# Optimization experiments

Measured on AMD Instinct MI355X. Metric: run time of the kernel, lower is better.

## Reference

```python
import jax, jax.numpy as jnp
import numpy as np

NUM_BASES = 8
DEGREE = 3
KSIZE = 3
DOMAIN = (0.0, 1.0)


def bspline_basis(x, degree, knots):
    """Cox-de Boor recursion, vectorized over all elements of x.
    x: [...] float; knots: [num_bases + degree + 1].
    Returns basis values of shape [..., num_bases].
    (The original torch code evaluates this same recursion per-tap inside
    nested loops; here it is evaluated once, batched, with correct knot
    index bookkeeping. Uniform distinct knots -> no zero denominators.)
    """
    xe = x[..., None]  # [..., 1]
    # degree-0: indicator of each knot interval -> [..., L-1]
    B = ((knots[:-1] <= xe) & (xe < knots[1:])).astype(x.dtype)
    for d in range(1, degree + 1):
        left = (xe - knots[:-(d + 1)]) / (knots[d:-1] - knots[:-(d + 1)]) * B[..., :-1]
        right = (knots[d + 1:] - xe) / (knots[d + 1:] - knots[1:-d]) * B[..., 1:]
        B = left + right  # [..., L-d-1]
    return B  # [..., num_bases]


def setup_inputs() -> dict:
    key = jax.random.key(0)
    k1, k2 = jax.random.split(key)
    # inputs uniform in [0,1) so they lie inside the B-spline domain
    x = jax.random.uniform(k1, (16, 64, 64, 64), dtype=jnp.float32)
    # per-tap spline coefficients: [Cout, Cin, K, K, num_bases]
    coeff = jax.random.normal(k2, (64, 64, KSIZE, KSIZE, NUM_BASES), dtype=jnp.float32)
    return {"x": x, "coeff": coeff}


def reference(x, coeff):
    # normalize to domain (identity for domain=(0,1), kept for faithfulness)
    xn = (x - DOMAIN[0]) / (DOMAIN[1] - DOMAIN[0])
    knots = jnp.linspace(DOMAIN[0], DOMAIN[1], NUM_BASES + DEGREE + 1, dtype=x.dtype)
    # spline basis for every input element: [B, Cin, H, W, nb]
    phi = bspline_basis(xn, DEGREE, knots)
    Bn, Cin, H, W, nb = phi.shape
    Cout = coeff.shape[0]
    # The KAN conv  out[b,o,h,w] = sum_{j,k,l,m} phi[b,j,h+k,w+l,m]*coeff[o,j,k,l,m]
    # is exactly a VALID conv with Cin*nb input channels.
    phi_c = jnp.transpose(phi, (0, 1, 4, 2, 3)).reshape(Bn, Cin * nb, H, W)
    w = jnp.transpose(coeff, (0, 1, 4, 2, 3)).reshape(Cout, Cin * nb, KSIZE, KSIZE)
    out = jax.lax.conv_general_dilated(
        phi_c, w, window_strides=(1, 1), padding="VALID",
        dimension_numbers=("NCHW", "OIHW", "NCHW"))
    return out  # [B, Cout, H-K+1, W-K+1]
```

## Files before the change

### kernel.cpp

```cpp
#include <hip/hip_runtime.h>
#include <hip/hip_bf16.h>


typedef short v8s __attribute__((ext_vector_type(8)));
typedef float v4f __attribute__((ext_vector_type(4)));
typedef float v16f __attribute__((ext_vector_type(16)));
typedef unsigned long long u64;
typedef u64 v2u64 __attribute__((ext_vector_type(2)));

#define B_N   16
#define CIN   64
#define COUT  64
#define H_IN  64
#define W_IN  64
#define NB    8
#define HO    62
#define WO    62
#define JC    8
#define NCH   8

__device__ __forceinline__ ushort f2bf(float f) {
    uint xu = __float_as_uint(f);
    return (ushort)((xu + 0x7fffu + ((xu >> 16) & 1u)) >> 16);
}

__device__ __forceinline__ uint cvtpk(float a, float b) {
    uint r;
    asm("v_cvt_pk_bf16_f32 %0, %1, %2" : "=v"(r) : "v"(a), "v"(b));
    return r;
}

__global__ void prep_coeff_kernel(const float* __restrict__ coeff, ushort* __restrict__ bt) {
    int n = blockIdx.x * 256 + threadIdx.x;
    if (n >= 294912) return;
    int m  = n & 7;
    int g2 = (n >> 3) & 1;
    int o  = (n >> 4) & 63;
    int jp = (n >> 10) & 3;
    int q  = n >> 12;
    int tap = q % 9;
    int jc  = q / 9;
    int j = jc * 8 + jp * 2 + g2;
    bt[n] = f2bf(coeff[((o * CIN + j) * 9 + tap) * 8 + m]);
}

#define MFMA32(a, b, c) __builtin_amdgcn_mfma_f32_32x32x16_bf16((a), (b), (c), 0, 0, 0)
#define MFMA16(a, b, c) __builtin_amdgcn_mfma_f32_16x16x32_bf16((a), (b), (c), 0, 0, 0)

__global__ __launch_bounds__(256, 4) void kan_conv_ks3(
        const float* __restrict__ x, const ushort* __restrict__ cb,
        float* __restrict__ out) {
    const int h    = blockIdx.x;
    const int b    = blockIdx.y;
    const int tid  = threadIdx.x;
    const int lane = tid & 63;
    const int kh   = tid >> 6;
    const int l31  = lane & 31;
    const int g2   = lane >> 5;

    __shared__ __align__(16) char smraw[32768];

    char* wrB = smraw + kh * 6144 + lane * 16;
    const char* rdB = smraw + kh * 6144 + g2 * 1024 + l31 * 16;

    v16f acc[2][2];
    acc[0][0] = (v16f)(0.f); acc[0][1] = (v16f)(0.f);
    acc[1][0] = (v16f)(0.f); acc[1][1] = (v16f)(0.f);

    float xr0[6], xr1[6];
    const float* xb = x + ((size_t)(b * CIN) * H_IN + h) * W_IN + lane;
    const int jx = kh * 2;

#define XL(dst, jcn) { \
    _Pragma("unroll") \
    for (int e = 0; e < 6; ++e) \
        dst[e] = xb[(size_t)((jcn) * 8 + jx + (e & 1)) * (H_IN * W_IN) + (e >> 1) * W_IN]; \
    }

    auto PW = [&](float xval, int e) {
        float s_ = xval * 11.0f;
        int i0 = (int)s_;
        i0 = i0 < 0 ? 0 : (i0 > 10 ? 10 : i0);
        float u  = s_ - (float)i0;
        float um = 1.0f - u;
        float u2 = u * u, u3 = u2 * u;
        const float inv6 = 1.0f / 6.0f;
        float n0 = um * um * um * inv6;
        float n1 = (3.0f * u3 - 6.0f * u2 + 4.0f) * inv6;
        float n2 = (-3.0f * u3 + 3.0f * u2 + 3.0f * u + 1.0f) * inv6;
        float n3 = u3 * inv6;
        u64 V = (u64)cvtpk(n0, n1) | ((u64)cvtpk(n2, n3) << 32);
        int bi = i0 - 3;
        u64 lo = bi < 0 ? (V >> (uint)(-16 * bi))
               : bi < 4 ? (V << (uint)(16 * bi)) : 0ull;
        u64 hi = bi <= 0 ? 0ull
               : bi < 4 ? (V >> (uint)(64 - 16 * bi))
               : (V << (uint)(16 * bi - 64));
        v2u64 pk; pk[0] = lo; pk[1] = hi;
        *reinterpret_cast<v2u64*>(wrB + e * 1024) = pk;
    };
    auto TAP = [&](const char* pAc, int k, int lt, int tap) {
        v8s b0 = *reinterpret_cast<const v8s*>(rdB + k * 2048 + lt * 16);
        v8s b1 = *reinterpret_cast<const v8s*>(rdB + k * 2048 + 512 + lt * 16);
        v8s a0 = *reinterpret_cast<const v8s*>(pAc + tap * 8192);
        v8s a1 = *reinterpret_cast<const v8s*>(pAc + tap * 8192 + 1024);
        acc[0][0] = MFMA32(a0, b0, acc[0][0]);
        acc[0][1] = MFMA32(a0, b1, acc[0][1]);
        acc[1][0] = MFMA32(a1, b0, acc[1][0]);
        acc[1][1] = MFMA32(a1, b1, acc[1][1]);
    };

    const char* pA = (const char*)cb + (size_t)(kh * 128 + l31 * 2 + g2) * 16;

    XL(xr0, 0);
    PW(xr0[0], 0); PW(xr0[1], 1); PW(xr0[2], 2);
    PW(xr0[3], 3); PW(xr0[4], 4); PW(xr0[5], 5);
    XL(xr1, 1);

#define CHUNK(jc, CUR, NXT) { \
    const char* pAc = pA + (size_t)(jc) * 73728; \
    TAP(pAc, 0, 0, 0); \
    TAP(pAc, 0, 1, 1); \
    if ((jc) + 2 < NCH) XL(NXT, (jc) + 2); \
    TAP(pAc, 0, 2, 2); \
    if ((jc) + 1 < NCH) { PW(CUR[0], 0); PW(CUR[1], 1); } \
    TAP(pAc, 1, 0, 3); \
    TAP(pAc, 1, 1, 4); \
    TAP(pAc, 1, 2, 5); \
    if ((jc) + 1 < NCH) { PW(CUR[2], 2); PW(CUR[3], 3); } \
    TAP(pAc, 2, 0, 6); \
    TAP(pAc, 2, 1, 7); \
    TAP(pAc, 2, 2, 8); \
    if ((jc) + 1 < NCH) { PW(CUR[4], 4); PW(CUR[5], 5); } \
    }

    for (int jj = 0; jj < 4; ++jj) {
        CHUNK(2 * jj,     xr1, xr0);
        CHUNK(2 * jj + 1, xr0, xr1);
    }

#define WR_FULL(off) { \
    _Pragma("unroll") \
    for (int t = 0; t < 4; ++t) { \
        _Pragma("unroll") \
        for (int q = 0; q < 4; ++q) { \
            v4f v; \
            _Pragma("unroll") \
            for (int z = 0; z < 4; ++z) v[z] = acc[t >> 1][t & 1][q * 4 + z]; \
            *reinterpret_cast<v4f*>(smraw + (off) + (t * 4 + q) * 1024 + lane * 16) = v; \
        } } }
#define ADD_FULL(off) { \
    _Pragma("unroll") \
    for (int t = 0; t < 4; ++t) { \
        _Pragma("unroll") \
        for (int q = 0; q < 4; ++q) { \
            v4f v = *reinterpret_cast<const v4f*>(smraw + (off) + (t * 4 + q) * 1024 + lane * 16); \
            _Pragma("unroll") \
            for (int z = 0; z < 4; ++z) acc[t >> 1][t & 1][q * 4 + z] += v[z]; \
        } } }
#define WR_HALF(OT, off) { \
    _Pragma("unroll") \
    for (int wf = 0; wf < 2; ++wf) { \
        _Pragma("unroll") \
        for (int q = 0; q < 4; ++q) { \
            v4f v; \
            _Pragma("unroll") \
            for (int z = 0; z < 4; ++z) v[z] = acc[OT][wf][q * 4 + z]; \
            *reinterpret_cast<v4f*>(smraw + (off) + (wf * 4 + q) * 1024 + lane * 16) = v; \
        } } }
#define ADD_HALF(OT, off) { \
    _Pragma("unroll") \
    for (int wf = 0; wf < 2; ++wf) { \
        _Pragma("unroll") \
        for (int q = 0; q < 4; ++q) { \
            v4f v = *reinterpret_cast<const v4f*>(smraw + (off) + (wf * 4 + q) * 1024 + lane * 16); \
            _Pragma("unroll") \
            for (int z = 0; z < 4; ++z) acc[OT][wf][q * 4 + z] += v[z]; \
        } } }
#define STORE_HALF(OT) { \
    _Pragma("unroll") \
    for (int wf = 0; wf < 2; ++wf) { \
        int w = wf * 32 + l31; \
        if (w < WO) { \
            _Pragma("unroll") \
            for (int reg = 0; reg < 16; ++reg) { \
                int o = (OT) * 32 + (reg & 3) + 8 * (reg >> 2) + 4 * g2; \
                out[((b * COUT + o) * HO + h) * WO + w] = acc[OT][wf][reg]; \
            } } } }

    __syncthreads();
    if (kh == 1) WR_FULL(0);
    if (kh == 3) WR_FULL(16384);
    __syncthreads();
    if (kh == 0) ADD_FULL(0);
    if (kh == 2) ADD_FULL(16384);
    __syncthreads();
    if (kh == 2) WR_HALF(0, 0);
    if (kh == 0) WR_HALF(1, 8192);
    __syncthreads();
    if (kh == 0) { ADD_HALF(0, 0);    STORE_HALF(0); }
    if (kh == 2) { ADD_HALF(1, 8192); STORE_HALF(1); }
}

__global__ __launch_bounds__(256, 4) void kan_conv_fb(
        const float* __restrict__ x, const float* __restrict__ coeff_f,
        float* __restrict__ out) {
    const int h    = blockIdx.x;
    const int b    = blockIdx.y;
    const int tid  = threadIdx.x;
    const int lane = tid & 63;
    const int wv   = tid >> 6;
    const int g    = lane >> 4;
    const int l15  = lane & 15;
    const int obase = (wv >> 1) << 5;
    const int wbase = (wv & 1) << 5;

    __shared__ __align__(16) ushort phi_lds[3 * JC * W_IN * NB];
    __shared__ uint lut[72];
    if (tid < 72) {
        int tap = tid;
        int j  = tap / 9;
        int r9 = tap - j * 9;
        int kt = r9 / 3;
        int lt = r9 - kt * 3;
        lut[tap] = (uint)(((kt * JC + j) * W_IN) * NB) | ((uint)lt << 16)
                 | ((uint)j << 20) | ((uint)r9 << 24);
    }
    v4f acc00 = {0.f, 0.f, 0.f, 0.f};
    v4f acc01 = acc00, acc10 = acc00, acc11 = acc00;
    const int aoff = obase + l15;
    float xv[6];
    #pragma unroll
    for (int it = 0; it < 6; ++it) {
        int n = it * 256 + tid;
        xv[it] = x[((b * CIN + ((n >> 6) & 7)) * H_IN + (h + (n >> 9))) * W_IN + (n & 63)];
    }
    for (int jc = 0; jc < NCH; ++jc) {
        #pragma unroll
        for (int it = 0; it < 6; ++it) {
            int n = it * 256 + tid;
            float s  = xv[it] * 11.0f;
            int i0 = (int)s;
            i0 = i0 < 0 ? 0 : (i0 > 10 ? 10 : i0);
            float u  = s - (float)i0;
            float um = 1.0f - u;
            float u2 = u * u, u3 = u2 * u;
            const float inv6 = 1.0f / 6.0f;
            float n0 = um * um * um * inv6;
            float n1 = (3.0f * u3 - 6.0f * u2 + 4.0f) * inv6;
            float n2 = (-3.0f * u3 + 3.0f * u2 + 3.0f * u + 1.0f) * inv6;
            float n3 = u3 * inv6;
            u64 V = (u64)f2bf(n0) | ((u64)f2bf(n1) << 16)
                  | ((u64)f2bf(n2) << 32) | ((u64)f2bf(n3) << 48);
            int bi = i0 - 3;
            u64 lo = bi < 0 ? (V >> (uint)(-16 * bi))
                   : bi < 4 ? (V << (uint)(16 * bi)) : 0ull;
            u64 hi = bi <= 0 ? 0ull
                   : bi < 4 ? (V >> (uint)(64 - 16 * bi))
                   : (V << (uint)(16 * bi - 64));
            v2u64 pk; pk[0] = lo; pk[1] = hi;
            *reinterpret_cast<v2u64*>(&phi_lds[n << 3]) = pk;
        }
        if (jc + 1 < NCH) {
            int j0n = (jc + 1) * JC;
            #pragma unroll
            for (int it = 0; it < 6; ++it) {
                int n = it * 256 + tid;
                xv[it] = x[((b * CIN + j0n + ((n >> 6) & 7)) * H_IN + (h + (n >> 9))) * W_IN + (n & 63)];
            }
        }
        __syncthreads();
        const int j0 = jc * JC;
        #pragma unroll 6
        for (int kk = 0; kk < 18; ++kk) {
            int tap = (kk << 2) + g;
            uint e = lut[tap];
            int philoc = (int)(e & 0xffffu);
            int lt     = (int)((e >> 16) & 3u);
            int w0 = wbase + l15 + lt;
            int w1 = w0 + 16;
            w0 = w0 < 63 ? w0 : 63;
            w1 = w1 < 63 ? w1 : 63;
            v8s pb0 = *reinterpret_cast<const v8s*>(&phi_lds[philoc + (w0 << 3)]);
            v8s pb1 = *reinterpret_cast<const v8s*>(&phi_lds[philoc + (w1 << 3)]);
            int j  = (int)((e >> 20) & 15u);
            int r9 = (int)((e >> 24) & 15u);
            const float* cf = coeff_f + (((aoff * CIN + (j0 + j)) * 9 + r9) << 3);
            v8s pa0, pa1;
            #pragma unroll
            for (int z = 0; z < 8; ++z) pa0[z] = (short)f2bf(cf[z]);
            const float* cf2 = cf + (CIN * 9 * NB * 16);
            #pragma unroll
            for (int z = 0; z < 8; ++z) pa1[z] = (short)f2bf(cf2[z]);
            acc00 = MFMA16(pa0, pb0, acc00);
            acc01 = MFMA16(pa0, pb1, acc01);
            acc10 = MFMA16(pa1, pb0, acc10);
            acc11 = MFMA16(pa1, pb1, acc11);
        }
        __syncthreads();
    }
    const int wc0 = wbase + l15;
    const int wc1 = wc0 + 16;
    #pragma unroll
    for (int i = 0; i < 2; ++i) {
        v4f a0 = (i == 0) ? acc00 : acc10;
        v4f a1 = (i == 0) ? acc01 : acc11;
        int o = obase + i * 16 + (g << 2);
        #pragma unroll
        for (int r = 0; r < 4; ++r) {
            int off = ((b * COUT + o + r) * HO + h) * WO;
            if (wc0 < WO) out[off + wc0] = a0[r];
            if (wc1 < WO) out[off + wc1] = a1[r];
        }
    }
}

extern "C" void kernel_launch(void* const* d_in, const int* in_sizes, int n_in,
                              void* d_out, int out_size, void* d_ws, size_t ws_size,
                              hipStream_t stream) {
    const float* x     = (const float*)d_in[0];
    const float* coeff = (const float*)d_in[1];
    float* out = (float*)d_out;

    const size_t bt_bytes = (size_t)294912 * 2;
    if (ws_size >= bt_bytes) {
        ushort* bt = (ushort*)d_ws;
        prep_coeff_kernel<<<(294912 + 255) / 256, 256, 0, stream>>>(coeff, bt);
        kan_conv_ks3<<<dim3(HO, B_N), 256, 0, stream>>>(x, bt, out);
    } else {
        kan_conv_fb<<<dim3(HO, B_N), 256, 0, stream>>>(x, coeff, out);
    }
}
```

Baseline: 53.44 us.

## Process two output rows per block with 512 threads sharing coefficient loads

```diff
diff --git a/kernel.cpp b/kernel.cpp
--- a/kernel.cpp
+++ b/kernel.cpp
@@ -47,28 +47,29 @@
 #define MFMA32(a, b, c) __builtin_amdgcn_mfma_f32_32x32x16_bf16((a), (b), (c), 0, 0, 0)
 #define MFMA16(a, b, c) __builtin_amdgcn_mfma_f32_16x16x32_bf16((a), (b), (c), 0, 0, 0)
 
-__global__ __launch_bounds__(256, 4) void kan_conv_ks3(
+__global__ __launch_bounds__(512, 4) void kan_conv_hp2(
         const float* __restrict__ x, const ushort* __restrict__ cb,
         float* __restrict__ out) {
-    const int h    = blockIdx.x;
+    extern __shared__ __align__(16) char smraw[];
+    const int h0   = blockIdx.x * 2;
     const int b    = blockIdx.y;
     const int tid  = threadIdx.x;
     const int lane = tid & 63;
-    const int kh   = tid >> 6;
+    const int wv   = tid >> 6;
+    const int kh   = wv & 3;
+    const int hh   = wv >> 2;
     const int l31  = lane & 31;
     const int g2   = lane >> 5;
 
-    __shared__ __align__(16) char smraw[32768];
-
-    char* wrB = smraw + kh * 6144 + lane * 16;
-    const char* rdB = smraw + kh * 6144 + g2 * 1024 + l31 * 16;
+    char* wrB = smraw + wv * 6144 + lane * 16;
+    const char* rdB = smraw + wv * 6144 + g2 * 1024 + l31 * 16;
 
     v16f acc[2][2];
     acc[0][0] = (v16f)(0.f); acc[0][1] = (v16f)(0.f);
     acc[1][0] = (v16f)(0.f); acc[1][1] = (v16f)(0.f);
 
     float xr0[6], xr1[6];
-    const float* xb = x + ((size_t)(b * CIN) * H_IN + h) * W_IN + lane;
+    const float* xb = x + ((size_t)(b * CIN) * H_IN + (h0 + hh)) * W_IN + lane;
     const int jx = kh * 2;
 
 #define XL(dst, jcn) { \
@@ -78,9 +79,8 @@
     }
 
     auto PW = [&](float xval, int e) {
-        float s_ = xval * 11.0f;
+        float s_ = fminf(fmaxf(xval * 11.0f, 0.0f), 10.999f);
         int i0 = (int)s_;
-        i0 = i0 < 0 ? 0 : (i0 > 10 ? 10 : i0);
         float u  = s_ - (float)i0;
         float um = 1.0f - u;
         float u2 = u * u, u3 = u2 * u;
@@ -119,18 +119,12 @@
 
 #define CHUNK(jc, CUR, NXT) { \
     const char* pAc = pA + (size_t)(jc) * 73728; \
-    TAP(pAc, 0, 0, 0); \
-    TAP(pAc, 0, 1, 1); \
     if ((jc) + 2 < NCH) XL(NXT, (jc) + 2); \
-    TAP(pAc, 0, 2, 2); \
+    TAP(pAc, 0, 0, 0); TAP(pAc, 0, 1, 1); TAP(pAc, 0, 2, 2); \
     if ((jc) + 1 < NCH) { PW(CUR[0], 0); PW(CUR[1], 1); } \
-    TAP(pAc, 1, 0, 3); \
-    TAP(pAc, 1, 1, 4); \
-    TAP(pAc, 1, 2, 5); \
+    TAP(pAc, 1, 0, 3); TAP(pAc, 1, 1, 4); TAP(pAc, 1, 2, 5); \
     if ((jc) + 1 < NCH) { PW(CUR[2], 2); PW(CUR[3], 3); } \
-    TAP(pAc, 2, 0, 6); \
-    TAP(pAc, 2, 1, 7); \
-    TAP(pAc, 2, 2, 8); \
+    TAP(pAc, 2, 0, 6); TAP(pAc, 2, 1, 7); TAP(pAc, 2, 2, 8); \
     if ((jc) + 1 < NCH) { PW(CUR[4], 4); PW(CUR[5], 5); } \
     }
 
@@ -185,21 +179,22 @@
             _Pragma("unroll") \
             for (int reg = 0; reg < 16; ++reg) { \
                 int o = (OT) * 32 + (reg & 3) + 8 * (reg >> 2) + 4 * g2; \
-                out[((b * COUT + o) * HO + h) * WO + w] = acc[OT][wf][reg]; \
+                out[((b * COUT + o) * HO + (h0 + hh)) * WO + w] = acc[OT][wf][reg]; \
             } } } }
 
+    const int ro = hh * 32768;
     __syncthreads();
-    if (kh == 1) WR_FULL(0);
-    if (kh == 3) WR_FULL(16384);
+    if (kh == 1) WR_FULL(ro);
+    if (kh == 3) WR_FULL(ro + 16384);
     __syncthreads();
-    if (kh == 0) ADD_FULL(0);
-    if (kh == 2) ADD_FULL(16384);
+    if (kh == 0) ADD_FULL(ro);
+    if (kh == 2) ADD_FULL(ro + 16384);
     __syncthreads();
-    if (kh == 2) WR_HALF(0, 0);
-    if (kh == 0) WR_HALF(1, 8192);
+    if (kh == 2) WR_HALF(0, ro);
+    if (kh == 0) WR_HALF(1, ro + 8192);
     __syncthreads();
-    if (kh == 0) { ADD_HALF(0, 0);    STORE_HALF(0); }
-    if (kh == 2) { ADD_HALF(1, 8192); STORE_HALF(1); }
+    if (kh == 0) { ADD_HALF(0, ro);        STORE_HALF(0); }
+    if (kh == 2) { ADD_HALF(1, ro + 8192); STORE_HALF(1); }
 }
 
 __global__ __launch_bounds__(256, 4) void kan_conv_fb(
@@ -326,7 +321,7 @@
     if (ws_size >= bt_bytes) {
         ushort* bt = (ushort*)d_ws;
         prep_coeff_kernel<<<(294912 + 255) / 256, 256, 0, stream>>>(coeff, bt);
-        kan_conv_ks3<<<dim3(HO, B_N), 256, 0, stream>>>(x, bt, out);
+        kan_conv_hp2<<<dim3(HO / 2, B_N), 512, 65536, stream>>>(x, bt, out);
     } else {
         kan_conv_fb<<<dim3(HO, B_N), 256, 0, stream>>>(x, coeff, out);
     }
```

Result: no change. 53.88 us (+0.8%).

## Software-pipeline coefficient fragment loads two taps ahead with rotating registers

Applied to the files above, without the earlier changes.

```diff
diff --git a/kernel.cpp b/kernel.cpp
--- a/kernel.cpp
+++ b/kernel.cpp
@@ -47,7 +47,7 @@
 #define MFMA32(a, b, c) __builtin_amdgcn_mfma_f32_32x32x16_bf16((a), (b), (c), 0, 0, 0)
 #define MFMA16(a, b, c) __builtin_amdgcn_mfma_f32_16x16x32_bf16((a), (b), (c), 0, 0, 0)
 
-__global__ __launch_bounds__(256, 4) void kan_conv_ks3(
+__global__ __launch_bounds__(256, 4) void kan_conv_pf(
         const float* __restrict__ x, const ushort* __restrict__ cb,
         float* __restrict__ out) {
     const int h    = blockIdx.x;
@@ -67,7 +67,7 @@
     acc[0][0] = (v16f)(0.f); acc[0][1] = (v16f)(0.f);
     acc[1][0] = (v16f)(0.f); acc[1][1] = (v16f)(0.f);
 
-    float xr0[6], xr1[6];
+    float xr[6];
     const float* xb = x + ((size_t)(b * CIN) * H_IN + h) * W_IN + lane;
     const int jx = kh * 2;
 
@@ -78,17 +78,17 @@
     }
 
     auto PW = [&](float xval, int e) {
-        float s_ = xval * 11.0f;
+        float s_ = fminf(fmaxf(xval * 11.0f, 0.0f), 10.999f);
         int i0 = (int)s_;
-        i0 = i0 < 0 ? 0 : (i0 > 10 ? 10 : i0);
         float u  = s_ - (float)i0;
-        float um = 1.0f - u;
+        float t  = 1.0f - u;
         float u2 = u * u, u3 = u2 * u;
+        float t3 = t * t * t;
         const float inv6 = 1.0f / 6.0f;
-        float n0 = um * um * um * inv6;
-        float n1 = (3.0f * u3 - 6.0f * u2 + 4.0f) * inv6;
-        float n2 = (-3.0f * u3 + 3.0f * u2 + 3.0f * u + 1.0f) * inv6;
+        float n0 = t3 * inv6;
         float n3 = u3 * inv6;
+        float n1 = fmaf(u2, fmaf(u, 0.5f, -1.0f), 2.0f / 3.0f);
+        float n2 = 1.0f - n0 - n1 - n3;
         u64 V = (u64)cvtpk(n0, n1) | ((u64)cvtpk(n2, n3) << 32);
         int bi = i0 - 3;
         u64 lo = bi < 0 ? (V >> (uint)(-16 * bi))
@@ -99,45 +99,49 @@
         v2u64 pk; pk[0] = lo; pk[1] = hi;
         *reinterpret_cast<v2u64*>(wrB + e * 1024) = pk;
     };
-    auto TAP = [&](const char* pAc, int k, int lt, int tap) {
-        v8s b0 = *reinterpret_cast<const v8s*>(rdB + k * 2048 + lt * 16);
-        v8s b1 = *reinterpret_cast<const v8s*>(rdB + k * 2048 + 512 + lt * 16);
-        v8s a0 = *reinterpret_cast<const v8s*>(pAc + tap * 8192);
-        v8s a1 = *reinterpret_cast<const v8s*>(pAc + tap * 8192 + 1024);
-        acc[0][0] = MFMA32(a0, b0, acc[0][0]);
-        acc[0][1] = MFMA32(a0, b1, acc[0][1]);
-        acc[1][0] = MFMA32(a1, b0, acc[1][0]);
-        acc[1][1] = MFMA32(a1, b1, acc[1][1]);
-    };
 
     const char* pA = (const char*)cb + (size_t)(kh * 128 + l31 * 2 + g2) * 16;
 
-    XL(xr0, 0);
-    PW(xr0[0], 0); PW(xr0[1], 1); PW(xr0[2], 2);
-    PW(xr0[3], 3); PW(xr0[4], 4); PW(xr0[5], 5);
-    XL(xr1, 1);
-
-#define CHUNK(jc, CUR, NXT) { \
+    v8s a0A, a1A, a0B, a1B, a0C, a1C;
+
+#define TAPR(k, lt, C0, C1, N0, N1, nptr) { \
+    v8s b0 = *reinterpret_cast<const v8s*>(rdB + (k) * 2048 + (lt) * 16); \
+    v8s b1 = *reinterpret_cast<const v8s*>(rdB + (k) * 2048 + 512 + (lt) * 16); \
+    N0 = *reinterpret_cast<const v8s*>(nptr); \
+    N1 = *reinterpret_cast<const v8s*>((nptr) + 1024); \
+    acc[0][0] = MFMA32(C0, b0, acc[0][0]); \
+    acc[0][1] = MFMA32(C0, b1, acc[0][1]); \
+    acc[1][0] = MFMA32(C1, b0, acc[1][0]); \
+    acc[1][1] = MFMA32(C1, b1, acc[1][1]); }
+
+#define CHUNKP(jc) { \
     const char* pAc = pA + (size_t)(jc) * 73728; \
-    TAP(pAc, 0, 0, 0); \
-    TAP(pAc, 0, 1, 1); \
-    if ((jc) + 2 < NCH) XL(NXT, (jc) + 2); \
-    TAP(pAc, 0, 2, 2); \
-    if ((jc) + 1 < NCH) { PW(CUR[0], 0); PW(CUR[1], 1); } \
-    TAP(pAc, 1, 0, 3); \
-    TAP(pAc, 1, 1, 4); \
-    TAP(pAc, 1, 2, 5); \
-    if ((jc) + 1 < NCH) { PW(CUR[2], 2); PW(CUR[3], 3); } \
-    TAP(pAc, 2, 0, 6); \
-    TAP(pAc, 2, 1, 7); \
-    TAP(pAc, 2, 2, 8); \
-    if ((jc) + 1 < NCH) { PW(CUR[4], 4); PW(CUR[5], 5); } \
-    }
-
-    for (int jj = 0; jj < 4; ++jj) {
-        CHUNK(2 * jj,     xr1, xr0);
-        CHUNK(2 * jj + 1, xr0, xr1);
-    }
+    const char* pAn = pA + (size_t)(((jc) + 1 < NCH) ? (jc) + 1 : 0) * 73728; \
+    if ((jc) + 1 < NCH) XL(xr, (jc) + 1); \
+    TAPR(0, 0, a0A, a1A, a0C, a1C, pAc + 2 * 8192); \
+    TAPR(0, 1, a0B, a1B, a0A, a1A, pAc + 3 * 8192); \
+    TAPR(0, 2, a0C, a1C, a0B, a1B, pAc + 4 * 8192); \
+    if ((jc) + 1 < NCH) { PW(xr[0], 0); PW(xr[1], 1); } \
+    TAPR(1, 0, a0A, a1A, a0C, a1C, pAc + 5 * 8192); \
+    TAPR(1, 1, a0B, a1B, a0A, a1A, pAc + 6 * 8192); \
+    TAPR(1, 2, a0C, a1C, a0B, a1B, pAc + 7 * 8192); \
+    if ((jc) + 1 < NCH) { PW(xr[2], 2); PW(xr[3], 3); } \
+    TAPR(2, 0, a0A, a1A, a0C, a1C, pAc + 8 * 8192); \
+    TAPR(2, 1, a0B, a1B, a0A, a1A, pAn + 0 * 8192); \
+    TAPR(2, 2, a0C, a1C, a0B, a1B, pAn + 1 * 8192); \
+    if ((jc) + 1 < NCH) { PW(xr[4], 4); PW(xr[5], 5); } \
+    }
+
+    XL(xr, 0);
+    PW(xr[0], 0); PW(xr[1], 1); PW(xr[2], 2);
+    PW(xr[3], 3); PW(xr[4], 4); PW(xr[5], 5);
+    a0A = *reinterpret_cast<const v8s*>(pA);
+    a1A = *reinterpret_cast<const v8s*>(pA + 1024);
+    a0B = *reinterpret_cast<const v8s*>(pA + 8192);
+    a1B = *reinterpret_cast<const v8s*>(pA + 8192 + 1024);
+
+    CHUNKP(0); CHUNKP(1); CHUNKP(2); CHUNKP(3);
+    CHUNKP(4); CHUNKP(5); CHUNKP(6); CHUNKP(7);
 
 #define WR_FULL(off) { \
     _Pragma("unroll") \
@@ -326,7 +330,7 @@
     if (ws_size >= bt_bytes) {
         ushort* bt = (ushort*)d_ws;
         prep_coeff_kernel<<<(294912 + 255) / 256, 256, 0, stream>>>(coeff, bt);
-        kan_conv_ks3<<<dim3(HO, B_N), 256, 0, stream>>>(x, bt, out);
+        kan_conv_pf<<<dim3(HO, B_N), 256, 0, stream>>>(x, bt, out);
     } else {
         kan_conv_fb<<<dim3(HO, B_N), 256, 0, stream>>>(x, coeff, out);
     }
```

Result: no change. 52.67 us (-1.4%).
